# Optimization experiments

Measured on AMD Instinct MI355X. Metric: run time of the kernel, lower is better.

## Reference

```python
import jax, jax.numpy as jnp
import numpy as np

D = 1024       # d_model
H = 16         # nhead
DFF = 4096     # dim_feedforward
TM = 512       # T_motion (seq_len)
TA = 512       # T_audio
B = 32         # batch
NBEATS = 64
SIGMA = 4.0    # temporal_sigma
BW = 2.0       # beat_weight
LN_EPS = 1e-5


def setup_inputs() -> dict:
    key = jax.random.key(0)
    ks = jax.random.split(key, 12)
    p = lambda k, shape: jax.random.normal(k, shape, jnp.float32) * 0.02
    return {
        "src": jax.random.normal(ks[0], (TM, B, D), jnp.float32),
        "audio_memory": jax.random.normal(ks[1], (TA, B, D), jnp.float32),
        "beat_frames": jax.random.randint(ks[2], (NBEATS,), 0, TA),
        # self-attention (packed in_proj like nn.MultiheadAttention)
        "sa_in_w": p(ks[3], (3 * D, D)), "sa_in_b": jnp.zeros((3 * D,), jnp.float32),
        "sa_out_w": p(ks[4], (D, D)), "sa_out_b": jnp.zeros((D,), jnp.float32),
        # cross-attention
        "ca_in_w": p(ks[5], (3 * D, D)), "ca_in_b": jnp.zeros((3 * D,), jnp.float32),
        "ca_out_w": p(ks[6], (D, D)), "ca_out_b": jnp.zeros((D,), jnp.float32),
        "gate": jnp.array(0.5, jnp.float32),  # cross_attn_gate (nonzero so branch is active)
        # layernorms
        "n1_g": jnp.ones((D,), jnp.float32), "n1_b": jnp.zeros((D,), jnp.float32),
        "nc_g": jnp.ones((D,), jnp.float32), "nc_b": jnp.zeros((D,), jnp.float32),
        "n2_g": jnp.ones((D,), jnp.float32), "n2_b": jnp.zeros((D,), jnp.float32),
        # FFN
        "lin1_w": p(ks[7], (DFF, D)), "lin1_b": jnp.zeros((DFF,), jnp.float32),
        "lin2_w": p(ks[8], (D, DFF)), "lin2_b": jnp.zeros((D,), jnp.float32),
    }


def _layernorm(x, g, b):
    m = jnp.mean(x, axis=-1, keepdims=True)
    v = jnp.var(x, axis=-1, keepdims=True)
    return (x - m) * jax.lax.rsqrt(v + LN_EPS) * g + b


def _mha(q, k, v, w_in, b_in, w_out, b_out, bias=None):
    # q: (Tq,B,D), k/v: (Tk,B,D); packed in_proj like nn.MultiheadAttention
    hd = D // H
    wq, wk, wv = jnp.split(w_in, 3, axis=0)
    bq, bk, bv = jnp.split(b_in, 3, axis=0)
    def proj(x, w, bb):  # (T,B,D) -> (B,H,T,hd)
        y = jnp.einsum('tbd,ed->tbe', x, w) + bb
        return y.reshape(y.shape[0], y.shape[1], H, hd).transpose(1, 2, 0, 3)
    qh, kh, vh = proj(q, wq, bq), proj(k, wk, bk), proj(v, wv, bv)
    scores = jnp.einsum('bhqd,bhkd->bhqk', qh, kh) / jnp.sqrt(jnp.float32(hd))
    if bias is not None:
        scores = scores + bias[None, None]  # (Tq,Tk) broadcast over (B,H)
    attn = jax.nn.softmax(scores, axis=-1)
    o = jnp.einsum('bhqk,bhkd->bhqd', attn, vh)          # (B,H,Tq,hd)
    o = o.transpose(2, 0, 1, 3).reshape(q.shape[0], q.shape[1], D)  # (Tq,B,D)
    return jnp.einsum('tbd,ed->tbe', o, w_out) + b_out


def _temporal_bias(t_motion, t_audio, sigma):
    scale = (t_audio - 1) / (t_motion - 1) if (t_motion > 1 and t_audio > 1) else 1.0
    audio_pos = jnp.arange(t_motion, dtype=jnp.float32) * scale
    diff = audio_pos[:, None] - jnp.arange(t_audio, dtype=jnp.float32)[None, :]
    return -(diff ** 2) / (2.0 * sigma ** 2)  # (T_motion, T_audio)


def _beat_bias(t_audio, beats, bw):
    # equivalent to sequential torch loop: beat position -> bw, neighbors -> max(., bw/2)
    bias = jnp.zeros((t_audio,), jnp.float32)
    l_idx = jnp.where(beats > 0, beats - 1, 0)
    l_val = jnp.where(beats > 0, bw * 0.5, 0.0)
    r_idx = jnp.where(beats < t_audio - 1, beats + 1, t_audio - 1)
    r_val = jnp.where(beats < t_audio - 1, bw * 0.5, 0.0)
    bias = bias.at[l_idx].max(l_val).at[r_idx].max(r_val).at[beats].max(bw)
    return bias


def reference(src, audio_memory, beat_frames, sa_in_w, sa_in_b, sa_out_w, sa_out_b,
              ca_in_w, ca_in_b, ca_out_w, ca_out_b, gate,
              n1_g, n1_b, nc_g, nc_b, n2_g, n2_b,
              lin1_w, lin1_b, lin2_w, lin2_b):
    # self-attention + residual + LN (dropout is identity in eval)
    x = src + _mha(src, src, src, sa_in_w, sa_in_b, sa_out_w, sa_out_b)
    x = _layernorm(x, n1_g, n1_b)
    # biased cross-attention to audio
    bias = _temporal_bias(TM, TA, SIGMA) + _beat_bias(TA, beat_frames, BW)[None, :]
    cross = _mha(x, audio_memory, audio_memory, ca_in_w, ca_in_b, ca_out_w, ca_out_b, bias)
    x = x + jnp.tanh(gate) * cross
    x = _layernorm(x, nc_g, nc_b)
    # FFN
    h = jax.nn.gelu(jnp.einsum('tbd,fd->tbf', x, lin1_w) + lin1_b, approximate=False)
    ff = jnp.einsum('tbf,df->tbd', h, lin2_w) + lin2_b
    x = _layernorm(x + ff, n2_g, n2_b)
    return x
```

## Files before the change

kernel.cpp:

```cpp
#include <hip/hip_runtime.h>
#include <hip/hip_bf16.h>

#define D_MODEL 1024
#define NHEAD   16
#define HDIM    64
#define DFF_    4096
#define TM_     512
#define TA_     512
#define BATCH   32
#define NTOK    (TM_ * BATCH)
#define NBEATS_ 64

typedef __bf16 bfv8 __attribute__((ext_vector_type(8)));
typedef float  f32x4 __attribute__((ext_vector_type(4)));
typedef unsigned short u16x8 __attribute__((ext_vector_type(8)));
typedef unsigned short u16x4 __attribute__((ext_vector_type(4)));

__device__ __forceinline__ unsigned short f2bf(float f) {
  union { float f; unsigned u; } v; v.f = f;
  unsigned r = v.u + 0x7fffu + ((v.u >> 16) & 1u);
  return (unsigned short)(r >> 16);
}
__device__ __forceinline__ float bf2f(unsigned short h) {
  union { unsigned u; float f; } v; v.u = ((unsigned)h) << 16;
  return v.f;
}
__device__ __forceinline__ unsigned pk2bf(float a, float b) {
  __hip_bfloat162 t = __float22bfloat162_rn(make_float2(a, b));
  union { __hip_bfloat162 h; unsigned u; } v; v.h = t;
  return v.u;
}
__device__ __forceinline__ float gelu_fast(float v) {
  float t = v * v;
  float e = __expf(v * fmaf(0.0713554f, t, 1.5957691f));
  float r = __builtin_amdgcn_rcpf(e + 1.0f);
  return v - v * r;
}

#define GLOAD_LDS16(g, l) __builtin_amdgcn_global_load_lds( \
    (const __attribute__((address_space(1))) unsigned int*)(g), \
    (__attribute__((address_space(3))) unsigned int*)(l), 16, 0, 0)

#define MEMFENCE asm volatile("" ::: "memory")
#define BARRIER  do { MEMFENCE; __builtin_amdgcn_s_barrier(); MEMFENCE; } while (0)

__global__ __launch_bounds__(256) void copy_f32(const float* __restrict__ in, float* __restrict__ out) {
  long i = ((long)blockIdx.x * 256 + threadIdx.x) * 4;
  *(float4*)(out + i) = *(const float4*)(in + i);
}

__global__ __launch_bounds__(256) void cvt_f32_bf16(
    const float* __restrict__ in, unsigned short* __restrict__ out) {
  long i = ((long)blockIdx.x * 256 + threadIdx.x) * 4;
  float4 v = *(const float4*)(in + i);
  u16x4 o = { f2bf(v.x), f2bf(v.y), f2bf(v.z), f2bf(v.w) };
  *(u16x4*)(out + i) = o;
}

__global__ __launch_bounds__(256) void cvt_remap_bt(
    const float* __restrict__ in, unsigned short* __restrict__ out) {
  long rin = blockIdx.x;
  int b = (int)(rin & 31), t = (int)(rin >> 5);
  long rout = (long)b * 512 + t;
  int c = threadIdx.x * 4;
  float4 v = *(const float4*)(in + rin * 1024 + c);
  u16x4 o = { f2bf(v.x), f2bf(v.y), f2bf(v.z), f2bf(v.w) };
  *(u16x4*)(out + rout * 1024 + c) = o;
}

__global__ __launch_bounds__(512) void build_biasT(
    const int* __restrict__ beats, float* __restrict__ biasT) {
  int ta = blockIdx.x;
  int tm = threadIdx.x;
  float m = 0.f;
  for (int i = 0; i < NBEATS_; ++i) {
    int bf = beats[i];
    if (bf == ta) m = fmaxf(m, 2.0f);
    if (bf > 0 && bf - 1 == ta) m = fmaxf(m, 1.0f);
    if (bf < TA_ - 1 && bf + 1 == ta) m = fmaxf(m, 1.0f);
  }
  float diff = (float)tm - (float)ta;
  biasT[ta * TM_ + tm] = -(diff * diff) * (1.0f / 32.0f) + m;
}

template<int EPI, int SWAP>
__global__ __launch_bounds__(512, 2) void gemm256p(
    const unsigned short* __restrict__ A, const unsigned short* __restrict__ Bw,
    const float* __restrict__ bias, int K,
    unsigned short* __restrict__ outP, int ldc,
    unsigned short* __restrict__ dq, unsigned short* __restrict__ dk,
    unsigned short* __restrict__ dv, int s1) {
  __shared__ __align__(16) unsigned short As[2][2][128 * 64];
  __shared__ __align__(16) unsigned short Bs[2][2][128 * 64];
  const int tid = threadIdx.x;
  const int w = tid >> 6, lane = tid & 63;
  const int l15 = lane & 15, l4 = lane >> 4;
  const int wm = w >> 2, wn = w & 3;
  const long m0 = (long)blockIdx.x * 256;
  const long n0 = (long)blockIdx.y * 256;
  const int srow8 = lane >> 3;
  const int scol = ((lane & 7) ^ srow8) * 8;

  const unsigned short* bA00 = A  + (m0 +       (w * 2 + 0) * 8 + srow8) * (long)K + scol;
  const unsigned short* bA01 = A  + (m0 +       (w * 2 + 1) * 8 + srow8) * (long)K + scol;
  const unsigned short* bA10 = A  + (m0 + 128 + (w * 2 + 0) * 8 + srow8) * (long)K + scol;
  const unsigned short* bA11 = A  + (m0 + 128 + (w * 2 + 1) * 8 + srow8) * (long)K + scol;
  const unsigned short* bB00 = Bw + (n0 +       (w * 2 + 0) * 8 + srow8) * (long)K + scol;
  const unsigned short* bB01 = Bw + (n0 +       (w * 2 + 1) * 8 + srow8) * (long)K + scol;
  const unsigned short* bB10 = Bw + (n0 + 128 + (w * 2 + 0) * 8 + srow8) * (long)K + scol;
  const unsigned short* bB11 = Bw + (n0 + 128 + (w * 2 + 1) * 8 + srow8) * (long)K + scol;

  auto stA = [&](int kt, int h, const unsigned short* p0, const unsigned short* p1) {
    const int db = kt & 1;
    const long ko = (long)kt * 64;
    GLOAD_LDS16(p0 + ko, &As[db][h][(w * 2 + 0) * 512]);
    GLOAD_LDS16(p1 + ko, &As[db][h][(w * 2 + 1) * 512]);
  };
  auto stB = [&](int kt, int h, const unsigned short* p0, const unsigned short* p1) {
    const int db = kt & 1;
    const long ko = (long)kt * 64;
    GLOAD_LDS16(p0 + ko, &Bs[db][h][(w * 2 + 0) * 512]);
    GLOAD_LDS16(p1 + ko, &Bs[db][h][(w * 2 + 1) * 512]);
  };
  const int swzb0 = ((l4)     ^ (l15 & 7)) << 4;
  const int swzb1 = ((l4 + 4) ^ (l15 & 7)) << 4;
  auto rdfrag = [&](const unsigned short* buf, int r, int kk) -> bfv8 {
    return *(const bfv8*)((const char*)buf + r * 128 + (kk ? swzb1 : swzb0));
  };

  f32x4 acc[8][4] = {};
  bfv8 aF[4][2], bF[4][2];
  const int nt = K >> 6;
  const int hB = wn >> 1, rB0 = (wn & 1) * 64;

  stA(0, 0, bA00, bA01); stA(0, 1, bA10, bA11);
  stB(0, 0, bB00, bB01); stB(0, 1, bB10, bB11);
  stB(1, 0, bB00, bB01); stB(1, 1, bB10, bB11);
  stA(1, 0, bA00, bA01); stA(1, 1, bA10, bA11);
  asm volatile("s_waitcnt vmcnt(8)" ::: "memory");
  BARRIER;

  for (int t = 0; t < nt; ++t) {
    const int db = t & 1;
    const unsigned short* Ah = &As[db][wm][0];
    const unsigned short* Bh = &Bs[db][hB][0];
    const bool pf2 = (t + 2 < nt);

#pragma unroll
    for (int mf = 0; mf < 4; ++mf) {
      aF[mf][0] = rdfrag(Ah, mf * 16 + l15, 0);
      aF[mf][1] = rdfrag(Ah, mf * 16 + l15, 1);
    }
#pragma unroll
    for (int nf = 0; nf < 2; ++nf) {
      bF[nf][0] = rdfrag(Bh, rB0 + nf * 16 + l15, 0);
      bF[nf][1] = rdfrag(Bh, rB0 + nf * 16 + l15, 1);
    }
    BARRIER;
    asm volatile("s_waitcnt lgkmcnt(0)" ::: "memory");
    __builtin_amdgcn_s_setprio(1);
#pragma unroll
    for (int mf = 0; mf < 4; ++mf)
#pragma unroll
      for (int nf = 0; nf < 2; ++nf)
#pragma unroll
        for (int kk = 0; kk < 2; ++kk)
          acc[mf][nf] = SWAP
            ? __builtin_amdgcn_mfma_f32_16x16x32_bf16(bF[nf][kk], aF[mf][kk], acc[mf][nf], 0, 0, 0)
            : __builtin_amdgcn_mfma_f32_16x16x32_bf16(aF[mf][kk], bF[nf][kk], acc[mf][nf], 0, 0, 0);
    __builtin_amdgcn_s_setprio(0);
    BARRIER;

#pragma unroll
    for (int nf = 2; nf < 4; ++nf) {
      bF[nf][0] = rdfrag(Bh, rB0 + nf * 16 + l15, 0);
      bF[nf][1] = rdfrag(Bh, rB0 + nf * 16 + l15, 1);
    }
    BARRIER;
    asm volatile("s_waitcnt lgkmcnt(0)" ::: "memory");
    __builtin_amdgcn_s_setprio(1);
#pragma unroll
    for (int mf = 0; mf < 4; ++mf)
#pragma unroll
      for (int nf = 2; nf < 4; ++nf)
#pragma unroll
        for (int kk = 0; kk < 2; ++kk)
          acc[mf][nf] = SWAP
            ? __builtin_amdgcn_mfma_f32_16x16x32_bf16(bF[nf][kk], aF[mf][kk], acc[mf][nf], 0, 0, 0)
            : __builtin_amdgcn_mfma_f32_16x16x32_bf16(aF[mf][kk], bF[nf][kk], acc[mf][nf], 0, 0, 0);
    __builtin_amdgcn_s_setprio(0);
    BARRIER;

#pragma unroll
    for (int mf = 0; mf < 4; ++mf) {
      aF[mf][0] = rdfrag(Ah, (mf + 4) * 16 + l15, 0);
      aF[mf][1] = rdfrag(Ah, (mf + 4) * 16 + l15, 1);
    }
    if (pf2) { stB(t + 2, 0, bB00, bB01); stB(t + 2, 1, bB10, bB11); }
    BARRIER;
    asm volatile("s_waitcnt lgkmcnt(0)" ::: "memory");
    __builtin_amdgcn_s_setprio(1);
#pragma unroll
    for (int mf = 0; mf < 4; ++mf)
#pragma unroll
      for (int nf = 0; nf < 2; ++nf)
#pragma unroll
        for (int kk = 0; kk < 2; ++kk)
          acc[mf + 4][nf] = SWAP
            ? __builtin_amdgcn_mfma_f32_16x16x32_bf16(bF[nf][kk], aF[mf][kk], acc[mf + 4][nf], 0, 0, 0)
            : __builtin_amdgcn_mfma_f32_16x16x32_bf16(aF[mf][kk], bF[nf][kk], acc[mf + 4][nf], 0, 0, 0);
    __builtin_amdgcn_s_setprio(0);
    BARRIER;

    if (pf2) { stA(t + 2, 0, bA00, bA01); stA(t + 2, 1, bA10, bA11); }
    __builtin_amdgcn_s_setprio(1);
#pragma unroll
    for (int mf = 0; mf < 4; ++mf)
#pragma unroll
      for (int nf = 2; nf < 4; ++nf)
#pragma unroll
        for (int kk = 0; kk < 2; ++kk)
          acc[mf + 4][nf] = SWAP
            ? __builtin_amdgcn_mfma_f32_16x16x32_bf16(bF[nf][kk], aF[mf][kk], acc[mf + 4][nf], 0, 0, 0)
            : __builtin_amdgcn_mfma_f32_16x16x32_bf16(aF[mf][kk], bF[nf][kk], acc[mf + 4][nf], 0, 0, 0);
    __builtin_amdgcn_s_setprio(0);
    if (pf2)                asm volatile("s_waitcnt vmcnt(8)" ::: "memory");
    else if (t + 1 < nt)    asm volatile("s_waitcnt vmcnt(0)" ::: "memory");
    BARRIER;
  }

#pragma unroll
  for (int mf = 0; mf < 8; ++mf)
#pragma unroll
    for (int nf = 0; nf < 4; ++nf) {
      if (SWAP) {
        const int mrow = (int)m0 + wm * 128 + mf * 16 + l15;
        const int col0 = (int)n0 + wn * 64 + nf * 16 + l4 * 4;
        float4 bv = bias ? *(const float4*)&bias[col0] : make_float4(0.f, 0.f, 0.f, 0.f);
        float v0 = acc[mf][nf][0] + bv.x, v1 = acc[mf][nf][1] + bv.y;
        float v2 = acc[mf][nf][2] + bv.z, v3 = acc[mf][nf][3] + bv.w;
        if (EPI == 1) { v0 = gelu_fast(v0); v1 = gelu_fast(v1); v2 = gelu_fast(v2); v3 = gelu_fast(v3); }
        if (EPI == 0 || EPI == 1) {
          uint2 ov; ov.x = pk2bf(v0, v1); ov.y = pk2bf(v2, v3);
          *(uint2*)&outP[(long)mrow * ldc + col0] = ov;
        } else {
          int b_ = mrow >> 9, t_ = mrow & 511;
          if (col0 < s1) {
            int h = col0 >> 6, d0 = col0 & 63;
            uint2 ov; ov.x = pk2bf(v0 * 0.125f, v1 * 0.125f); ov.y = pk2bf(v2 * 0.125f, v3 * 0.125f);
            *(uint2*)&dq[(((long)b_ * NHEAD + h) * TM_ + t_) * HDIM + d0] = ov;
          } else {
            int c0 = col0 - s1, h = c0 >> 6, d0 = c0 & 63;
            uint2 ov; ov.x = pk2bf(v0, v1); ov.y = pk2bf(v2, v3);
            *(uint2*)&dk[(((long)b_ * NHEAD + h) * TA_ + t_) * HDIM + d0] = ov;
          }
        }
      } else {
        const int col = (int)n0 + wn * 64 + nf * 16 + l15;
        const int row0 = (int)m0 + wm * 128 + mf * 16 + l4 * 4;
        float bv = bias ? bias[col] : 0.f;
        int b_ = row0 >> 9, t0 = row0 & 511;
        int h = col >> 6, d = col & 63;
        uint2 ov;
        ov.x = pk2bf(acc[mf][nf][0] + bv, acc[mf][nf][1] + bv);
        ov.y = pk2bf(acc[mf][nf][2] + bv, acc[mf][nf][3] + bv);
        *(uint2*)&dv[(((long)b_ * NHEAD + h) * HDIM + d) * TA_ + t0] = ov;
      }
    }
}

template<int BIAS>
__global__ __launch_bounds__(256) void attn_fused5(
    const unsigned short* __restrict__ Qr, const unsigned short* __restrict__ Kr,
    const unsigned short* __restrict__ Vt, const float* __restrict__ biasT,
    unsigned short* __restrict__ Orow) {
  __shared__ __align__(16) unsigned short Kb[2][64 * 64];
  __shared__ __align__(16) unsigned short Vb[2][64 * 64];
  __shared__ __align__(16) unsigned short P_lds[4][16][64];
  const int flat = blockIdx.y * 8 + blockIdx.x;
  const int W = (flat & 7) * 512 + (flat >> 3);
  const int bh = W >> 3;
  const int b = bh >> 4, h = bh & 15;
  const int tid = threadIdx.x, w = tid >> 6, lane = tid & 63;
  const int l15 = lane & 15, l4 = lane >> 4;
  const int q0 = (W & 7) * 64 + w * 16;

  const unsigned short* Kg = Kr + (long)bh * TA_ * HDIM;
  const unsigned short* Vg = Vt + (long)bh * HDIM * TA_;

  const int stg_row = w * 8 + (lane >> 3);
  const int stg_col = ((lane & 7) ^ (lane >> 3)) * 8;

  auto stage = [&](int t, int cb) {
    const int kv0 = t * 64;
#pragma unroll
    for (int i = 0; i < 2; ++i) {
      int row = i * 32 + stg_row;
      GLOAD_LDS16(Kg + (long)(kv0 + row) * HDIM + stg_col, &Kb[cb][(i * 32 + w * 8) * 64]);
      GLOAD_LDS16(Vg + (long)row * TA_ + kv0 + stg_col,    &Vb[cb][(i * 32 + w * 8) * 64]);
    }
  };

  bfv8 qf[2];
#pragma unroll
  for (int kc = 0; kc < 2; ++kc)
    qf[kc] = *(const bfv8*)&Qr[((long)bh * TM_ + q0 + l15) * HDIM + kc * 32 + l4 * 8];

  float mrun = -1e30f, lrun = 0.f;
  f32x4 o[4] = {};
  unsigned short* prow = &P_lds[w][l15][0];
  const int swz = (l15 & 7) * 8;

  stage(0, 0);
  __syncthreads();
  int cur = 0;

  for (int t = 0; t < 8; ++t) {
    if (t < 7) stage(t + 1, cur ^ 1);
    const int kv0 = t * 64;
    f32x4 s[4] = {};
#pragma unroll
    for (int f = 0; f < 4; ++f) {
#pragma unroll
      for (int kc = 0; kc < 2; ++kc) {
        bfv8 kf = *(const bfv8*)&Kb[cur][(f * 16 + l15) * 64 + (((kc * 4 + l4) * 8) ^ swz)];
        s[f] = __builtin_amdgcn_mfma_f32_16x16x32_bf16(kf, qf[kc], s[f], 0, 0, 0);
      }
    }
    if (BIAS) {
#pragma unroll
      for (int f = 0; f < 4; ++f)
#pragma unroll
        for (int r = 0; r < 4; ++r)
          s[f][r] += biasT[(long)(kv0 + f * 16 + l4 * 4 + r) * TM_ + q0 + l15];
    }
    float tmx = -1e30f;
#pragma unroll
    for (int f = 0; f < 4; ++f)
#pragma unroll
      for (int r = 0; r < 4; ++r) tmx = fmaxf(tmx, s[f][r]);
    tmx = fmaxf(tmx, __shfl_xor(tmx, 16));
    tmx = fmaxf(tmx, __shfl_xor(tmx, 32));
    float newm = fmaxf(mrun, tmx);
    float corr = __expf(mrun - newm);
    lrun *= corr;
#pragma unroll
    for (int fd = 0; fd < 4; ++fd)
#pragma unroll
      for (int r = 0; r < 4; ++r) o[fd][r] *= corr;
    float psum = 0.f;
#pragma unroll
    for (int f = 0; f < 4; ++f) {
#pragma unroll
      for (int r = 0; r < 4; ++r) { float e = __expf(s[f][r] - newm); s[f][r] = e; psum += e; }
      unsigned p0 = pk2bf(s[f][0], s[f][1]);
      unsigned p1 = pk2bf(s[f][2], s[f][3]);
      int blkW = ((f << 1) | (l4 >> 1)) ^ (l15 & 7);
      uint2 pw; pw.x = p0; pw.y = p1;
      *(uint2*)((char*)prow + blkW * 16 + (l4 & 1) * 8) = pw;
    }
    psum += __shfl_xor(psum, 16);
    psum += __shfl_xor(psum, 32);
    lrun += psum;
    mrun = newm;
    asm volatile("s_waitcnt lgkmcnt(0)" ::: "memory");
    __builtin_amdgcn_sched_barrier(0);
#pragma unroll
    for (int c = 0; c < 2; ++c) {
      int blkR = ((c << 2) | l4) ^ (l15 & 7);
      bfv8 pa = *(const bfv8*)((const char*)prow + blkR * 16);
#pragma unroll
      for (int fd = 0; fd < 4; ++fd) {
        bfv8 vb = *(const bfv8*)&Vb[cur][(fd * 16 + l15) * 64 + (((c * 4 + l4) * 8) ^ swz)];
        o[fd] = __builtin_amdgcn_mfma_f32_16x16x32_bf16(vb, pa, o[fd], 0, 0, 0);
      }
    }
    __syncthreads();
    cur ^= 1;
  }

  float invl = 1.f / lrun;
  const long obase = ((long)b * 512 + q0 + l15) * D_MODEL + h * HDIM;
#pragma unroll
  for (int fd = 0; fd < 4; ++fd) {
    uint2 ov;
    ov.x = pk2bf(o[fd][0] * invl, o[fd][1] * invl);
    ov.y = pk2bf(o[fd][2] * invl, o[fd][3] * invl);
    *(uint2*)&Orow[obase + fd * 16 + l4 * 4] = ov;
  }
}

__global__ __launch_bounds__(256) void ln_fused(
    const unsigned short* __restrict__ cin,
    const float* __restrict__ residf, const unsigned short* __restrict__ residb,
    const float* __restrict__ gamma, const float* __restrict__ beta,
    const float* __restrict__ gate,
    float* __restrict__ out_f32, unsigned short* __restrict__ out_bf16,
    int remap_resid, int remap_out) {
  long row = blockIdx.x;
  int t = threadIdx.x;
  int tt = (int)(row & 511), bb = (int)(row >> 9);
  long row_tb = (long)tt * 32 + bb;
  float gf = gate ? tanhf(gate[0]) : 1.0f;
  u16x4 cvb = *(const u16x4*)(cin + row * 1024 + t * 4);
  float c0 = bf2f(cvb[0]), c1 = bf2f(cvb[1]), c2 = bf2f(cvb[2]), c3 = bf2f(cvb[3]);
  float r0, r1, r2, r3;
  if (residf) {
    long rr = remap_resid ? row_tb : row;
    float4 rv = *(const float4*)(residf + rr * 1024 + t * 4);
    r0 = rv.x; r1 = rv.y; r2 = rv.z; r3 = rv.w;
  } else {
    u16x4 rv = *(const u16x4*)(residb + row * 1024 + t * 4);
    r0 = bf2f(rv[0]); r1 = bf2f(rv[1]); r2 = bf2f(rv[2]); r3 = bf2f(rv[3]);
  }
  float y0 = r0 + gf * c0, y1 = r1 + gf * c1, y2 = r2 + gf * c2, y3 = r3 + gf * c3;
  float s = y0 + y1 + y2 + y3;
  float q = y0 * y0 + y1 * y1 + y2 * y2 + y3 * y3;
#pragma unroll
  for (int off = 32; off; off >>= 1) { s += __shfl_xor(s, off); q += __shfl_xor(q, off); }
  __shared__ float sw[4], qw[4];
  int wave = t >> 6;
  if ((t & 63) == 0) { sw[wave] = s; qw[wave] = q; }
  __syncthreads();
  s = sw[0] + sw[1] + sw[2] + sw[3];
  q = qw[0] + qw[1] + qw[2] + qw[3];
  float mean = s * (1.0f / 1024.0f);
  float var = q * (1.0f / 1024.0f) - mean * mean;
  float rstd = rsqrtf(var + 1e-5f);
  float4 g4 = *(const float4*)(gamma + t * 4);
  float4 b4 = *(const float4*)(beta + t * 4);
  float o0 = (y0 - mean) * rstd * g4.x + b4.x;
  float o1 = (y1 - mean) * rstd * g4.y + b4.y;
  float o2 = (y2 - mean) * rstd * g4.z + b4.z;
  float o3 = (y3 - mean) * rstd * g4.w + b4.w;
  if (out_f32) {
    long ro = remap_out ? row_tb : row;
    float4 o = { o0, o1, o2, o3 };
    *(float4*)(out_f32 + ro * 1024 + t * 4) = o;
  }
  if (out_bf16) {
    u16x4 ob = { f2bf(o0), f2bf(o1), f2bf(o2), f2bf(o3) };
    *(u16x4*)(out_bf16 + row * 1024 + t * 4) = ob;
  }
}

static inline char* wsa(char*& p, size_t bytes) {
  char* r = p;
  p += (bytes + 255) & ~(size_t)255;
  return r;
}

extern "C" void kernel_launch(void* const* d_in, const int* in_sizes, int n_in,
                              void* d_out, int out_size, void* d_ws, size_t ws_size,
                              hipStream_t stream) {
  const float* src      = (const float*)d_in[0];
  const float* audio    = (const float*)d_in[1];
  const int*   beats    = (const int*)d_in[2];
  const float* sa_in_w  = (const float*)d_in[3];
  const float* sa_in_b  = (const float*)d_in[4];
  const float* sa_out_w = (const float*)d_in[5];
  const float* sa_out_b = (const float*)d_in[6];
  const float* ca_in_w  = (const float*)d_in[7];
  const float* ca_in_b  = (const float*)d_in[8];
  const float* ca_out_w = (const float*)d_in[9];
  const float* ca_out_b = (const float*)d_in[10];
  const float* gate     = (const float*)d_in[11];
  const float* n1_g     = (const float*)d_in[12];
  const float* n1_b     = (const float*)d_in[13];
  const float* nc_g     = (const float*)d_in[14];
  const float* nc_b     = (const float*)d_in[15];
  const float* n2_g     = (const float*)d_in[16];
  const float* n2_b     = (const float*)d_in[17];
  const float* l1_w     = (const float*)d_in[18];
  const float* l1_b     = (const float*)d_in[19];
  const float* l2_w     = (const float*)d_in[20];
  const float* l2_b     = (const float*)d_in[21];
  float* out = (float*)d_out;
  (void)in_sizes; (void)n_in; (void)out_size;

  const size_t NEEDED = (size_t)236000000;
  if (ws_size < NEEDED) {
    copy_f32<<<dim3(NTOK), dim3(256), 0, stream>>>(src, out);
    return;
  }

  char* p = (char*)d_ws;
  float*          biasT  = (float*)         wsa(p, (size_t)TM_ * TA_ * 4);
  unsigned short* wsaiw  = (unsigned short*)wsa(p, (size_t)3 * D_MODEL * D_MODEL * 2);
  unsigned short* wsaow  = (unsigned short*)wsa(p, (size_t)D_MODEL * D_MODEL * 2);
  unsigned short* wcaiw  = (unsigned short*)wsa(p, (size_t)3 * D_MODEL * D_MODEL * 2);
  unsigned short* wcaow  = (unsigned short*)wsa(p, (size_t)D_MODEL * D_MODEL * 2);
  unsigned short* wl1    = (unsigned short*)wsa(p, (size_t)DFF_ * D_MODEL * 2);
  unsigned short* wl2    = (unsigned short*)wsa(p, (size_t)D_MODEL * DFF_ * 2);
  unsigned short* srcb   = (unsigned short*)wsa(p, (size_t)NTOK * D_MODEL * 2);
  unsigned short* audb   = (unsigned short*)wsa(p, (size_t)NTOK * D_MODEL * 2);
  unsigned short* Qr     = (unsigned short*)wsa(p, (size_t)NTOK * D_MODEL * 2);
  unsigned short* Kr     = (unsigned short*)wsa(p, (size_t)NTOK * D_MODEL * 2);
  unsigned short* Vt     = (unsigned short*)wsa(p, (size_t)NTOK * D_MODEL * 2);
  unsigned short* x1b    = (unsigned short*)wsa(p, (size_t)NTOK * D_MODEL * 2);
  unsigned short* Orow   = srcb;
  unsigned short* C1     = Vt;
  unsigned short* x2b    = audb;
  unsigned short* H1     = Qr;
  unsigned short* C2     = srcb;

  build_biasT<<<dim3(TA_), dim3(TM_), 0, stream>>>(beats, biasT);
  cvt_remap_bt<<<dim3(NTOK), dim3(256), 0, stream>>>(src, srcb);
  cvt_remap_bt<<<dim3(NTOK), dim3(256), 0, stream>>>(audio, audb);
  cvt_f32_bf16<<<dim3((3 * D_MODEL * D_MODEL) / 1024), dim3(256), 0, stream>>>(sa_in_w, wsaiw);
  cvt_f32_bf16<<<dim3((D_MODEL * D_MODEL) / 1024), dim3(256), 0, stream>>>(sa_out_w, wsaow);
  cvt_f32_bf16<<<dim3((3 * D_MODEL * D_MODEL) / 1024), dim3(256), 0, stream>>>(ca_in_w, wcaiw);
  cvt_f32_bf16<<<dim3((D_MODEL * D_MODEL) / 1024), dim3(256), 0, stream>>>(ca_out_w, wcaow);
  cvt_f32_bf16<<<dim3((DFF_ * D_MODEL) / 1024), dim3(256), 0, stream>>>(l1_w, wl1);
  cvt_f32_bf16<<<dim3((D_MODEL * DFF_) / 1024), dim3(256), 0, stream>>>(l2_w, wl2);

  gemm256p<3, 1><<<dim3(64, 8), dim3(512), 0, stream>>>(
      srcb, wsaiw, sa_in_b, 1024, nullptr, 0, Qr, Kr, nullptr, 1024);
  gemm256p<2, 0><<<dim3(64, 4), dim3(512), 0, stream>>>(
      srcb, wsaiw + (size_t)2048 * D_MODEL, sa_in_b + 2048, 1024,
      nullptr, 0, nullptr, nullptr, Vt, 0);
  attn_fused5<0><<<dim3(TM_ / 64, BATCH * NHEAD), dim3(256), 0, stream>>>(Qr, Kr, Vt, nullptr, Orow);
  gemm256p<0, 1><<<dim3(64, 4), dim3(512), 0, stream>>>(
      Orow, wsaow, sa_out_b, 1024, C1, 1024, nullptr, nullptr, nullptr, 0);
  ln_fused<<<dim3(NTOK), dim3(256), 0, stream>>>(
      C1, src, nullptr, n1_g, n1_b, nullptr, nullptr, x1b, 1, 0);

  gemm256p<3, 1><<<dim3(64, 4), dim3(512), 0, stream>>>(
      x1b, wcaiw, ca_in_b, 1024, nullptr, 0, Qr, nullptr, nullptr, 1024);
  gemm256p<3, 1><<<dim3(64, 4), dim3(512), 0, stream>>>(
      audb, wcaiw + (size_t)1024 * D_MODEL, ca_in_b + 1024, 1024,
      nullptr, 0, nullptr, Kr, nullptr, 0);
  gemm256p<2, 0><<<dim3(64, 4), dim3(512), 0, stream>>>(
      audb, wcaiw + (size_t)2048 * D_MODEL, ca_in_b + 2048, 1024,
      nullptr, 0, nullptr, nullptr, Vt, 0);
  attn_fused5<1><<<dim3(TM_ / 64, BATCH * NHEAD), dim3(256), 0, stream>>>(Qr, Kr, Vt, biasT, Orow);
  gemm256p<0, 1><<<dim3(64, 4), dim3(512), 0, stream>>>(
      Orow, wcaow, ca_out_b, 1024, C1, 1024, nullptr, nullptr, nullptr, 0);
  ln_fused<<<dim3(NTOK), dim3(256), 0, stream>>>(
      C1, nullptr, x1b, nc_g, nc_b, gate, nullptr, x2b, 0, 0);

  gemm256p<1, 1><<<dim3(64, 16), dim3(512), 0, stream>>>(
      x2b, wl1, l1_b, 1024, H1, DFF_, nullptr, nullptr, nullptr, 0);
  gemm256p<0, 1><<<dim3(64, 4), dim3(512), 0, stream>>>(
      H1, wl2, l2_b, DFF_, C2, 1024, nullptr, nullptr, nullptr, 0);
  ln_fused<<<dim3(NTOK), dim3(256), 0, stream>>>(
      C2, nullptr, x2b, n2_g, n2_b, nullptr, out, nullptr, 0, 1);
}
```

Baseline: 1.049 ms.

## Read V fragments from global directly and skip softmax rescale lazily

```diff
diff --git a/kernel.cpp b/kernel.cpp
--- a/kernel.cpp
+++ b/kernel.cpp
@@ -270,12 +270,11 @@
 }
 
 template<int BIAS>
-__global__ __launch_bounds__(256) void attn_fused5(
+__global__ __launch_bounds__(256) void attn_fused6(
     const unsigned short* __restrict__ Qr, const unsigned short* __restrict__ Kr,
     const unsigned short* __restrict__ Vt, const float* __restrict__ biasT,
     unsigned short* __restrict__ Orow) {
   __shared__ __align__(16) unsigned short Kb[2][64 * 64];
-  __shared__ __align__(16) unsigned short Vb[2][64 * 64];
   __shared__ __align__(16) unsigned short P_lds[4][16][64];
   const int flat = blockIdx.y * 8 + blockIdx.x;
   const int W = (flat & 7) * 512 + (flat >> 3);
@@ -297,7 +296,6 @@
     for (int i = 0; i < 2; ++i) {
       int row = i * 32 + stg_row;
       GLOAD_LDS16(Kg + (long)(kv0 + row) * HDIM + stg_col, &Kb[cb][(i * 32 + w * 8) * 64]);
-      GLOAD_LDS16(Vg + (long)row * TA_ + kv0 + stg_col,    &Vb[cb][(i * 32 + w * 8) * 64]);
     }
   };
 
@@ -334,35 +332,39 @@
         for (int r = 0; r < 4; ++r)
           s[f][r] += biasT[(long)(kv0 + f * 16 + l4 * 4 + r) * TM_ + q0 + l15];
     }
-    float tmx = -1e30f;
-#pragma unroll
-    for (int f = 0; f < 4; ++f)
-#pragma unroll
-      for (int r = 0; r < 4; ++r) tmx = fmaxf(tmx, s[f][r]);
-    tmx = fmaxf(tmx, __shfl_xor(tmx, 16));
-    tmx = fmaxf(tmx, __shfl_xor(tmx, 32));
-    float newm = fmaxf(mrun, tmx);
-    float corr = __expf(mrun - newm);
-    lrun *= corr;
-#pragma unroll
-    for (int fd = 0; fd < 4; ++fd)
-#pragma unroll
-      for (int r = 0; r < 4; ++r) o[fd][r] *= corr;
-    float psum = 0.f;
+    float t0 = fmaxf(fmaxf(s[0][0], s[0][1]), fmaxf(s[0][2], s[0][3]));
+    float t1 = fmaxf(fmaxf(s[1][0], s[1][1]), fmaxf(s[1][2], s[1][3]));
+    float t2 = fmaxf(fmaxf(s[2][0], s[2][1]), fmaxf(s[2][2], s[2][3]));
+    float t3 = fmaxf(fmaxf(s[3][0], s[3][1]), fmaxf(s[3][2], s[3][3]));
+    float pmax = fmaxf(fmaxf(t0, t1), fmaxf(t2, t3));
+    pmax = fmaxf(pmax, __shfl_xor(pmax, 16));
+    pmax = fmaxf(pmax, __shfl_xor(pmax, 32));
+    if (!__all(pmax - mrun <= 8.0f)) {
+      float newm = fmaxf(mrun, pmax);
+      float corr = __expf(mrun - newm);
+      lrun *= corr;
+#pragma unroll
+      for (int fd = 0; fd < 4; ++fd)
+#pragma unroll
+        for (int r = 0; r < 4; ++r) o[fd][r] *= corr;
+      mrun = newm;
+    }
+    float p0 = 0.f, p1 = 0.f, p2 = 0.f, p3 = 0.f;
 #pragma unroll
     for (int f = 0; f < 4; ++f) {
-#pragma unroll
-      for (int r = 0; r < 4; ++r) { float e = __expf(s[f][r] - newm); s[f][r] = e; psum += e; }
-      unsigned p0 = pk2bf(s[f][0], s[f][1]);
-      unsigned p1 = pk2bf(s[f][2], s[f][3]);
+      float e0 = __expf(s[f][0] - mrun), e1 = __expf(s[f][1] - mrun);
+      float e2 = __expf(s[f][2] - mrun), e3 = __expf(s[f][3] - mrun);
+      p0 += e0; p1 += e1; p2 += e2; p3 += e3;
+      unsigned w0 = pk2bf(e0, e1);
+      unsigned w1 = pk2bf(e2, e3);
       int blkW = ((f << 1) | (l4 >> 1)) ^ (l15 & 7);
-      uint2 pw; pw.x = p0; pw.y = p1;
+      uint2 pw; pw.x = w0; pw.y = w1;
       *(uint2*)((char*)prow + blkW * 16 + (l4 & 1) * 8) = pw;
     }
+    float psum = (p0 + p1) + (p2 + p3);
     psum += __shfl_xor(psum, 16);
     psum += __shfl_xor(psum, 32);
     lrun += psum;
-    mrun = newm;
     asm volatile("s_waitcnt lgkmcnt(0)" ::: "memory");
     __builtin_amdgcn_sched_barrier(0);
 #pragma unroll
@@ -371,7 +373,7 @@
       bfv8 pa = *(const bfv8*)((const char*)prow + blkR * 16);
 #pragma unroll
       for (int fd = 0; fd < 4; ++fd) {
-        bfv8 vb = *(const bfv8*)&Vb[cur][(fd * 16 + l15) * 64 + (((c * 4 + l4) * 8) ^ swz)];
+        bfv8 vb = *(const bfv8*)&Vg[(long)(fd * 16 + l15) * TA_ + kv0 + c * 32 + l4 * 8];
         o[fd] = __builtin_amdgcn_mfma_f32_16x16x32_bf16(vb, pa, o[fd], 0, 0, 0);
       }
     }
@@ -519,7 +521,7 @@
   gemm256p<2, 0><<<dim3(64, 4), dim3(512), 0, stream>>>(
       srcb, wsaiw + (size_t)2048 * D_MODEL, sa_in_b + 2048, 1024,
       nullptr, 0, nullptr, nullptr, Vt, 0);
-  attn_fused5<0><<<dim3(TM_ / 64, BATCH * NHEAD), dim3(256), 0, stream>>>(Qr, Kr, Vt, nullptr, Orow);
+  attn_fused6<0><<<dim3(TM_ / 64, BATCH * NHEAD), dim3(256), 0, stream>>>(Qr, Kr, Vt, nullptr, Orow);
   gemm256p<0, 1><<<dim3(64, 4), dim3(512), 0, stream>>>(
       Orow, wsaow, sa_out_b, 1024, C1, 1024, nullptr, nullptr, nullptr, 0);
   ln_fused<<<dim3(NTOK), dim3(256), 0, stream>>>(
@@ -533,7 +535,7 @@
   gemm256p<2, 0><<<dim3(64, 4), dim3(512), 0, stream>>>(
       audb, wcaiw + (size_t)2048 * D_MODEL, ca_in_b + 2048, 1024,
       nullptr, 0, nullptr, nullptr, Vt, 0);
-  attn_fused5<1><<<dim3(TM_ / 64, BATCH * NHEAD), dim3(256), 0, stream>>>(Qr, Kr, Vt, biasT, Orow);
+  attn_fused6<1><<<dim3(TM_ / 64, BATCH * NHEAD), dim3(256), 0, stream>>>(Qr, Kr, Vt, biasT, Orow);
   gemm256p<0, 1><<<dim3(64, 4), dim3(512), 0, stream>>>(
       Orow, wcaow, ca_out_b, 1024, C1, 1024, nullptr, nullptr, nullptr, 0);
   ln_fused<<<dim3(NTOK), dim3(256), 0, stream>>>(
```

New measurement: 1.185 ms. 1.13x slower.
